# Kernel tuning notes

Measured on AMD Instinct MI355X. Metric: run time of the kernel, lower is better.

The kernel has to match this reference:

```python
import jax, jax.numpy as jnp
import numpy as np

N = 200000   # num atoms (nodes)
E = 400000   # one-way edges; symmetrized to 2E inside forward
H = 256      # hidden_dim == hidden_feats
LN_EPS = 1e-5


def setup_inputs() -> dict:
    key = jax.random.key(0)
    ks = jax.random.split(key, 48)
    def p(i, shape, s=0.05):
        return jax.random.normal(ks[i], shape, dtype=jnp.float32) * s
    inp = {
        'atom_inputs': jax.random.randint(ks[0], (N, 7), 0, 2),
        'src': jax.random.randint(ks[1], (E,), 0, N),
        'dst': jax.random.randint(ks[2], (E,), 0, N),
        # AtomEmbedding tables
        'emb_element': p(3, (100, 64)),
        'emb_degree': p(4, (7, 4)),
        'emb_valence': p(5, (7, 4)),
        'emb_charge': p(6, (8, 4)),
        'emb_aromatic': p(7, (2, 4)),
        'emb_hybrid': p(8, (6, 4)),
        'emb_hydrogen': p(9, (5, 4)),
        # linear_0: 88 -> H
        'W0': p(10, (88, H)), 'b0': jnp.zeros((H,), jnp.float32),
        # linear_1: H -> H
        'W1': p(11, (H, H)), 'b1': jnp.zeros((H,), jnp.float32),
    }
    # 4 GINEConv layers: node-MLP weight Wn/bn, edge Linear(1,H) weight We/be,
    # followed by LayerNorm gamma g / beta bt
    for i in range(4):
        inp[f'Wn{i}'] = p(12 + 4 * i, (H, H))
        inp[f'bn{i}'] = jnp.zeros((H,), jnp.float32)
        inp[f'We{i}'] = p(13 + 4 * i, (H,))
        inp[f'be{i}'] = jnp.zeros((H,), jnp.float32)
        inp[f'g{i}'] = jnp.ones((H,), jnp.float32)
        inp[f'bt{i}'] = jnp.zeros((H,), jnp.float32)
    return inp


def _layernorm(x, g, b):
    m = jnp.mean(x, axis=-1, keepdims=True)
    v = jnp.mean(jnp.square(x - m), axis=-1, keepdims=True)
    return (x - m) / jnp.sqrt(v + LN_EPS) * g + b


def reference(atom_inputs, src, dst,
              emb_element, emb_degree, emb_valence, emb_charge,
              emb_aromatic, emb_hybrid, emb_hydrogen,
              W0, b0, W1, b1,
              Wn0, bn0, We0, be0, g0, bt0,
              Wn1, bn1, We1, be1, g1, bt1,
              Wn2, bn2, We2, be2, g2, bt2,
              Wn3, bn3, We3, be3, g3, bt3):
    # --- AtomEmbedding: 7 lookups, concat -> [N, 88]
    feats = jnp.concatenate([
        emb_element[atom_inputs[:, 0]],
        emb_degree[atom_inputs[:, 1]],
        emb_valence[atom_inputs[:, 2] + 1],
        emb_charge[atom_inputs[:, 3]],
        emb_aromatic[atom_inputs[:, 4]],
        emb_hybrid[atom_inputs[:, 5]],
        emb_hydrogen[atom_inputs[:, 6]],
    ], axis=-1)
    h = feats @ W0 + b0  # [N, H]
    n = h.shape[0]

    # symmetrize edges: src||dst -> dst||src
    s = jnp.concatenate([src, dst])
    d = jnp.concatenate([dst, src])

    def gine(x, Wn, bn, We, be):
        # edge_attr is all-ones [2E,1]; Linear(1,H) applied to ones is the
        # constant vector We + be broadcast over edges.
        c = We + be                                   # [H]
        msg = jax.nn.relu(x[s] + c)                   # [2E, H] gather + add
        agg = jax.ops.segment_sum(msg, d, num_segments=n)  # scatter-sum
        return (x + agg) @ Wn + bn                    # eps=0: (1+eps)*x + agg

    h = _layernorm(gine(h, Wn0, bn0, We0, be0), g0, bt0)
    h = _layernorm(gine(h, Wn1, bn1, We1, be1), g1, bt1)
    h = _layernorm(gine(h, Wn2, bn2, We2, be2), g2, bt2)
    h = _layernorm(gine(h, Wn3, bn3, We3, be3), g3, bt3)
    return h @ W1 + b1
```

## Files before the change

kernel.cpp:

```cpp
#include <hip/hip_runtime.h>

#define HDIM 256

typedef __attribute__((ext_vector_type(8))) short short8;
typedef __attribute__((ext_vector_type(4))) float f32x4;

typedef const __attribute__((address_space(1))) unsigned int* gas_ptr;
typedef __attribute__((address_space(3))) unsigned int* las_ptr;

__device__ __forceinline__ unsigned short f2bf(float f) {
    unsigned int u = __float_as_uint(f);
    u += 0x7FFF + ((u >> 16) & 1);
    return (unsigned short)(u >> 16);
}
__device__ __forceinline__ float bf2f(unsigned short u) {
    return __uint_as_float(((unsigned int)u) << 16);
}


__global__ void k_zero_int(int* p, int n) {
    int i = blockIdx.x * blockDim.x + threadIdx.x;
    if (i < n) p[i] = 0;
}

__global__ void k_hist(const int* __restrict__ src, const int* __restrict__ dst,
                       int E, int* __restrict__ deg) {
    int e = blockIdx.x * blockDim.x + threadIdx.x;
    if (e >= E) return;
    atomicAdd(&deg[dst[e]], 1);
    atomicAdd(&deg[src[e]], 1);
}

__global__ void k_scan_partial(const int* __restrict__ deg, int* __restrict__ rp,
                               int* __restrict__ bsum, int n) {
    __shared__ int sd[256];
    int t = threadIdx.x;
    int base = blockIdx.x * 1024 + t * 4;
    int v[4]; int tsum = 0;
    #pragma unroll
    for (int k = 0; k < 4; k++) { v[k] = (base + k < n) ? deg[base + k] : 0; tsum += v[k]; }
    sd[t] = tsum; __syncthreads();
    for (int off = 1; off < 256; off <<= 1) {
        int x = (t >= off) ? sd[t - off] : 0;
        __syncthreads();
        sd[t] += x;
        __syncthreads();
    }
    int run = sd[t] - tsum;
    if (t == 255) bsum[blockIdx.x] = sd[255];
    #pragma unroll
    for (int k = 0; k < 4; k++) { if (base + k < n) rp[base + k] = run; run += v[k]; }
}

__global__ void k_scan_bsum(int* __restrict__ bsum, int nb) {
    __shared__ int sd[256];
    int t = threadIdx.x;
    int base = t * 4;
    int v[4]; int tsum = 0;
    #pragma unroll
    for (int k = 0; k < 4; k++) { v[k] = (base + k < nb) ? bsum[base + k] : 0; tsum += v[k]; }
    sd[t] = tsum; __syncthreads();
    for (int off = 1; off < 256; off <<= 1) {
        int x = (t >= off) ? sd[t - off] : 0;
        __syncthreads();
        sd[t] += x;
        __syncthreads();
    }
    int run = sd[t] - tsum;
    #pragma unroll
    for (int k = 0; k < 4; k++) { if (base + k < nb) bsum[base + k] = run; run += v[k]; }
}

__global__ void k_scan_add(int* __restrict__ rp, int* __restrict__ cursor,
                           const int* __restrict__ bsum, int n, int twoE) {
    int i = blockIdx.x * blockDim.x + threadIdx.x;
    if (i < n) {
        int v = rp[i] + bsum[i >> 10];
        rp[i] = v;
        cursor[i] = v;
    }
    if (i == 0) rp[n] = twoE;
}

__global__ void k_fill(const int* __restrict__ src, const int* __restrict__ dst,
                       int E, int* __restrict__ cursor, int* __restrict__ col) {
    int e = blockIdx.x * blockDim.x + threadIdx.x;
    if (e >= E) return;
    int s = src[e], d = dst[e];
    int p = atomicAdd(&cursor[d], 1); col[p] = s;
    int q = atomicAdd(&cursor[s], 1); col[q] = d;
}


__global__ void k_prep_w(const float* __restrict__ W, unsigned short* __restrict__ Wt) {
    int k = blockIdx.x, nn = threadIdx.x;
    Wt[nn * 256 + k] = f2bf(W[k * 256 + nn]);
}

__global__ void k_prep_w0(const float* __restrict__ W0, unsigned short* __restrict__ Wt0) {
    int k = blockIdx.x, nn = threadIdx.x;
    Wt0[nn * 96 + k] = (k < 88) ? f2bf(W0[k * 256 + nn]) : 0;
}


__global__ __launch_bounds__(256) void k_embed0(
    const int* __restrict__ atom,
    const float* __restrict__ eE, const float* __restrict__ eD,
    const float* __restrict__ eV, const float* __restrict__ eC,
    const float* __restrict__ eA, const float* __restrict__ eH,
    const float* __restrict__ eHy,
    const unsigned short* __restrict__ Wt0, const float* __restrict__ b0,
    unsigned short* __restrict__ x, int n) {
    __shared__ __align__(128) unsigned short As[64 * 256];
    int t = threadIdx.x;
    size_t node0 = (size_t)blockIdx.x * 64;

    {
        int row = t >> 2;
        int ks  = (t & 3) * 24;
        size_t node = node0 + row;
        int a0 = 0, a1 = 0, a2 = 0, a3 = 0, a4 = 0, a5 = 0, a6 = 0;
        bool ok = node < (size_t)n;
        if (ok) {
            const int* a = atom + node * 7;
            a0 = a[0]; a1 = a[1]; a2 = a[2]; a3 = a[3]; a4 = a[4]; a5 = a[5]; a6 = a[6];
        }
        #pragma unroll
        for (int kk = 0; kk < 24; kk++) {
            int k = ks + kk;
            float val = 0.f;
            if (ok) {
                if (k < 64)       val = eE[a0 * 64 + k];
                else if (k < 68)  val = eD[a1 * 4 + (k - 64)];
                else if (k < 72)  val = eV[(a2 + 1) * 4 + (k - 68)];
                else if (k < 76)  val = eC[a3 * 4 + (k - 72)];
                else if (k < 80)  val = eA[a4 * 4 + (k - 76)];
                else if (k < 84)  val = eH[a5 * 4 + (k - 80)];
                else if (k < 88)  val = eHy[a6 * 4 + (k - 84)];
            }
            int boff = (k * 2) ^ ((row & 7) << 4);
            *(unsigned short*)((char*)As + row * 256 + boff) = f2bf(val);
        }
    }
    __syncthreads();

    int w  = t >> 6;
    int l  = t & 63;
    int lr = l & 15;
    int lk = l >> 4;

    f32x4 acc[4][4];
    #pragma unroll
    for (int rg = 0; rg < 4; rg++)
        #pragma unroll
        for (int cg = 0; cg < 4; cg++)
            acc[rg][cg] = (f32x4){0.f, 0.f, 0.f, 0.f};

    #pragma unroll
    for (int kt = 0; kt < 3; kt++) {
        int kbyte = kt * 64 + lk * 16;
        short8 a[4], bf[4];
        #pragma unroll
        for (int rg = 0; rg < 4; rg++) {
            int row = rg * 16 + lr;
            a[rg] = *(const short8*)((const char*)As + row * 256 + (kbyte ^ ((row & 7) << 4)));
        }
        #pragma unroll
        for (int cg = 0; cg < 4; cg++) {
            int coln = w * 64 + cg * 16 + lr;
            bf[cg] = *(const short8*)((const char*)Wt0 + coln * 192 + kbyte);
        }
        #pragma unroll
        for (int rg = 0; rg < 4; rg++)
            #pragma unroll
            for (int cg = 0; cg < 4; cg++)
                acc[rg][cg] = __builtin_amdgcn_mfma_f32_16x16x32_bf16(a[rg], bf[cg], acc[rg][cg], 0, 0, 0);
    }

    float bcol[4];
    #pragma unroll
    for (int cg = 0; cg < 4; cg++) bcol[cg] = b0[w * 64 + cg * 16 + lr];

    __syncthreads();
    #pragma unroll
    for (int rg = 0; rg < 4; rg++)
        #pragma unroll
        for (int j = 0; j < 4; j++) {
            int row = rg * 16 + lk * 4 + j;
            #pragma unroll
            for (int cg = 0; cg < 4; cg++) {
                int colI = w * 64 + cg * 16 + lr;
                int byte = row * 512 + ((((colI >> 2) << 3) ^ ((row & 7) << 4)) + (colI & 3) * 2);
                *(unsigned short*)((char*)As + byte) = f2bf(acc[rg][cg][j] + bcol[cg]);
            }
        }
    __syncthreads();
    ushort4* xo = (ushort4*)(x + node0 * HDIM);
    #pragma unroll
    for (int i = 0; i < 16; i++) {
        int g4 = i * 256 + t;
        int row = g4 >> 6, c4 = g4 & 63;
        if (node0 + row < (size_t)n)
            xo[g4] = *(ushort4*)((char*)As + row * 512 + ((c4 << 3) ^ ((row & 7) << 4)));
    }
}


__global__ __launch_bounds__(256) void k_aggregate(
    const unsigned short* __restrict__ x, const int* __restrict__ rp,
    const int* __restrict__ col, const float* __restrict__ We,
    const float* __restrict__ be, unsigned short* __restrict__ z, int n) {
    int wid = threadIdx.x >> 6;
    int l   = threadIdx.x & 63;
    int h   = l >> 5;
    int j   = l & 31;
    int node = blockIdx.x * 8 + wid * 2 + h;
    bool ok = node < n;
    int nd = ok ? node : 0;
    const short8* x8 = (const short8*)x;

    float c[8];
    {
        float4 w0 = ((const float4*)We)[2 * j],     w1 = ((const float4*)We)[2 * j + 1];
        float4 e0 = ((const float4*)be)[2 * j],     e1 = ((const float4*)be)[2 * j + 1];
        c[0] = w0.x + e0.x; c[1] = w0.y + e0.y; c[2] = w0.z + e0.z; c[3] = w0.w + e0.w;
        c[4] = w1.x + e1.x; c[5] = w1.y + e1.y; c[6] = w1.z + e1.z; c[7] = w1.w + e1.w;
    }

    int p0 = rp[nd], p1 = rp[nd + 1];
    int deg = ok ? (p1 - p0) : 0;

    float acc[8];
    {
        short8 s = x8[(size_t)nd * 32 + j];
        #pragma unroll
        for (int k = 0; k < 8; k++) acc[k] = ok ? bf2f((unsigned short)s[k]) : 0.f;
    }

    for (int b = 0; b < deg; b += 32) {
        int m = deg - b; if (m > 32) m = 32;
        int idx = (j < m) ? col[p0 + b + j] : 0;
        int e = 0;
        for (; e + 2 <= m; e += 2) {
            int s0 = __shfl(idx, (h << 5) + e, 64);
            int s1 = __shfl(idx, (h << 5) + e + 1, 64);
            short8 u0 = x8[(size_t)s0 * 32 + j];
            short8 u1 = x8[(size_t)s1 * 32 + j];
            #pragma unroll
            for (int k = 0; k < 8; k++) acc[k] += fmaxf(bf2f((unsigned short)u0[k]) + c[k], 0.f);
            #pragma unroll
            for (int k = 0; k < 8; k++) acc[k] += fmaxf(bf2f((unsigned short)u1[k]) + c[k], 0.f);
        }
        if (e < m) {
            int s0 = __shfl(idx, (h << 5) + e, 64);
            short8 u0 = x8[(size_t)s0 * 32 + j];
            #pragma unroll
            for (int k = 0; k < 8; k++) acc[k] += fmaxf(bf2f((unsigned short)u0[k]) + c[k], 0.f);
        }
    }

    if (ok) {
        short8 o;
        #pragma unroll
        for (int k = 0; k < 8; k++) o[k] = (short)f2bf(acc[k]);
        ((short8*)z)[(size_t)nd * 32 + j] = o;
    }
}


template <bool DO_LN>
__global__ __launch_bounds__(256) void k_gemm_mfma(
    const unsigned short* __restrict__ zin, const unsigned short* __restrict__ Wt,
    const float* __restrict__ b, const float* __restrict__ g,
    const float* __restrict__ bt, void* __restrict__ xout_v, int n) {
    __shared__ __align__(128) unsigned short As[64 * 256];
    __shared__ float psum[4][64], psq[4][64];
    __shared__ float mean_s[64], inv_s[64];

    int t = threadIdx.x;
    int w = t >> 6;
    int l = t & 63;
    size_t node0 = (size_t)blockIdx.x * 64;

    if (node0 + 64 <= (size_t)n) {
        const char* ztile = (const char*)(zin + node0 * HDIM);
        #pragma unroll
        for (int it = 0; it < 8; it++) {
            int ldsbase = w * 8192 + it * 1024;
            int row = (ldsbase >> 9) + (l >> 5);
            int chunk = (l & 31) * 16;
            const char* src = ztile + row * 512 + (chunk ^ ((row & 7) << 4));
            __builtin_amdgcn_global_load_lds((gas_ptr)src,
                                             (las_ptr)((char*)As + ldsbase),
                                             16, 0, 0);
        }
    } else {
        const ushort4* zr = (const ushort4*)(zin + node0 * HDIM);
        #pragma unroll
        for (int i = 0; i < 16; i++) {
            int g4 = i * 256 + t;
            int row = g4 >> 6, c4 = g4 & 63;
            ushort4 v = make_ushort4(0, 0, 0, 0);
            if (node0 + row < (size_t)n) v = zr[g4];
            *(ushort4*)((char*)As + row * 512 + ((c4 << 3) ^ ((row & 7) << 4))) = v;
        }
    }
    __syncthreads();

    int lr = l & 15;
    int lk = l >> 4;

    f32x4 acc[4][4];
    #pragma unroll
    for (int rg = 0; rg < 4; rg++)
        #pragma unroll
        for (int cg = 0; cg < 4; cg++)
            acc[rg][cg] = (f32x4){0.f, 0.f, 0.f, 0.f};

    #pragma unroll
    for (int kt = 0; kt < 8; kt++) {
        int kbyte = kt * 64 + lk * 16;
        short8 a[4], bf[4];
        #pragma unroll
        for (int rg = 0; rg < 4; rg++) {
            int row = rg * 16 + lr;
            a[rg] = *(const short8*)((const char*)As + row * 512 + (kbyte ^ ((row & 7) << 4)));
        }
        #pragma unroll
        for (int cg = 0; cg < 4; cg++) {
            int coln = w * 64 + cg * 16 + lr;
            bf[cg] = *(const short8*)((const char*)Wt + coln * 512 + kbyte);
        }
        #pragma unroll
        for (int rg = 0; rg < 4; rg++)
            #pragma unroll
            for (int cg = 0; cg < 4; cg++)
                acc[rg][cg] = __builtin_amdgcn_mfma_f32_16x16x32_bf16(a[rg], bf[cg], acc[rg][cg], 0, 0, 0);
    }

    float bcol[4];
    #pragma unroll
    for (int cg = 0; cg < 4; cg++) bcol[cg] = b[w * 64 + cg * 16 + lr];
    #pragma unroll
    for (int rg = 0; rg < 4; rg++)
        #pragma unroll
        for (int cg = 0; cg < 4; cg++)
            #pragma unroll
            for (int j = 0; j < 4; j++) acc[rg][cg][j] += bcol[cg];

    if (!DO_LN) {
        float* xout = (float*)xout_v;
        #pragma unroll
        for (int rg = 0; rg < 4; rg++)
            #pragma unroll
            for (int j = 0; j < 4; j++) {
                int row = rg * 16 + lk * 4 + j;
                size_t node = node0 + row;
                if (node < (size_t)n) {
                    #pragma unroll
                    for (int cg = 0; cg < 4; cg++)
                        xout[node * HDIM + w * 64 + cg * 16 + lr] = acc[rg][cg][j];
                }
            }
        return;
    }

    float sv[4][4], sq[4][4];
    #pragma unroll
    for (int rg = 0; rg < 4; rg++)
        #pragma unroll
        for (int j = 0; j < 4; j++) {
            float s = 0.f, q = 0.f;
            #pragma unroll
            for (int cg = 0; cg < 4; cg++) {
                float v = acc[rg][cg][j];
                s += v; q += v * v;
            }
            sv[rg][j] = s; sq[rg][j] = q;
        }
    #pragma unroll
    for (int off = 1; off < 16; off <<= 1) {
        #pragma unroll
        for (int rg = 0; rg < 4; rg++)
            #pragma unroll
            for (int j = 0; j < 4; j++) {
                sv[rg][j] += __shfl_xor(sv[rg][j], off, 64);
                sq[rg][j] += __shfl_xor(sq[rg][j], off, 64);
            }
    }
    if (lr == 0) {
        #pragma unroll
        for (int rg = 0; rg < 4; rg++)
            #pragma unroll
            for (int j = 0; j < 4; j++) {
                int row = rg * 16 + lk * 4 + j;
                psum[w][row] = sv[rg][j];
                psq[w][row]  = sq[rg][j];
            }
    }
    __syncthreads();
    if (t < 64) {
        float s = psum[0][t] + psum[1][t] + psum[2][t] + psum[3][t];
        float q = psq[0][t] + psq[1][t] + psq[2][t] + psq[3][t];
        float m = s * (1.f / 256.f);
        float var = q * (1.f / 256.f) - m * m;
        mean_s[t] = m;
        inv_s[t]  = rsqrtf(var + 1e-5f);
    }
    __syncthreads();

    float gv[4], btv[4];
    #pragma unroll
    for (int cg = 0; cg < 4; cg++) {
        int coln = w * 64 + cg * 16 + lr;
        gv[cg] = g[coln]; btv[cg] = bt[coln];
    }
    #pragma unroll
    for (int rg = 0; rg < 4; rg++)
        #pragma unroll
        for (int j = 0; j < 4; j++) {
            int row = rg * 16 + lk * 4 + j;
            float m = mean_s[row];
            float inv = inv_s[row];
            #pragma unroll
            for (int cg = 0; cg < 4; cg++) {
                int colI = w * 64 + cg * 16 + lr;
                float v = (acc[rg][cg][j] - m) * inv * gv[cg] + btv[cg];
                int byte = row * 512 + ((((colI >> 2) << 3) ^ ((row & 7) << 4)) + (colI & 3) * 2);
                *(unsigned short*)((char*)As + byte) = f2bf(v);
            }
        }
    __syncthreads();
    ushort4* xo = (ushort4*)((unsigned short*)xout_v + node0 * HDIM);
    #pragma unroll
    for (int i = 0; i < 16; i++) {
        int g4 = i * 256 + t;
        int row = g4 >> 6, c4 = g4 & 63;
        if (node0 + row < (size_t)n)
            xo[g4] = *(ushort4*)((char*)As + row * 512 + ((c4 << 3) ^ ((row & 7) << 4)));
    }
}


extern "C" void kernel_launch(void* const* d_in, const int* in_sizes, int n_in,
                              void* d_out, int out_size, void* d_ws, size_t ws_size,
                              hipStream_t stream) {
    const int*   atom = (const int*)d_in[0];
    const int*   src  = (const int*)d_in[1];
    const int*   dst  = (const int*)d_in[2];
    const float* eE   = (const float*)d_in[3];
    const float* eD   = (const float*)d_in[4];
    const float* eV   = (const float*)d_in[5];
    const float* eC   = (const float*)d_in[6];
    const float* eA   = (const float*)d_in[7];
    const float* eH   = (const float*)d_in[8];
    const float* eHy  = (const float*)d_in[9];
    const float* W0   = (const float*)d_in[10];
    const float* b0   = (const float*)d_in[11];
    const float* W1   = (const float*)d_in[12];
    const float* b1   = (const float*)d_in[13];

    const int N = in_sizes[0] / 7;
    const int E = in_sizes[1];
    const int twoE = 2 * E;

    unsigned short* xb = (unsigned short*)d_ws;
    unsigned short* z  = xb + (size_t)N * HDIM;
    int*   rp      = (int*)(z + (size_t)N * HDIM);
    int*   cursor  = rp + (N + 1);
    int*   deg     = cursor + N;
    int*   col     = deg + N;
    int*   bsum    = col + twoE;
    uintptr_t pw = (uintptr_t)(bsum + 1024);
    pw = (pw + 255) & ~(uintptr_t)255;
    unsigned short* Wt  = (unsigned short*)pw;
    unsigned short* Wt0 = Wt + (size_t)5 * 65536;

    const int nb = (N + 1023) / 1024;

    k_zero_int<<<(N + 255) / 256, 256, 0, stream>>>(deg, N);
    k_hist<<<(E + 255) / 256, 256, 0, stream>>>(src, dst, E, deg);
    k_scan_partial<<<nb, 256, 0, stream>>>(deg, rp, bsum, N);
    k_scan_bsum<<<1, 256, 0, stream>>>(bsum, nb);
    k_scan_add<<<(N + 255) / 256, 256, 0, stream>>>(rp, cursor, bsum, N, twoE);
    k_fill<<<(E + 255) / 256, 256, 0, stream>>>(src, dst, E, cursor, col);

    for (int L = 0; L < 4; L++) {
        const float* Wn = (const float*)d_in[14 + 6 * L + 0];
        k_prep_w<<<256, 256, 0, stream>>>(Wn, Wt + (size_t)L * 65536);
    }
    k_prep_w<<<256, 256, 0, stream>>>(W1, Wt + (size_t)4 * 65536);
    k_prep_w0<<<96, 256, 0, stream>>>(W0, Wt0);

    const int nblk64 = (N + 63) / 64;
    const int nblk8  = (N + 7) / 8;

    k_embed0<<<nblk64, 256, 0, stream>>>(atom, eE, eD, eV, eC, eA, eH, eHy,
                                         Wt0, b0, xb, N);

    for (int L = 0; L < 4; L++) {
        const float* bn = (const float*)d_in[14 + 6 * L + 1];
        const float* We = (const float*)d_in[14 + 6 * L + 2];
        const float* be = (const float*)d_in[14 + 6 * L + 3];
        const float* g  = (const float*)d_in[14 + 6 * L + 4];
        const float* bt = (const float*)d_in[14 + 6 * L + 5];
        k_aggregate<<<nblk8, 256, 0, stream>>>(xb, rp, col, We, be, z, N);
        k_gemm_mfma<true><<<nblk64, 256, 0, stream>>>(z, Wt + (size_t)L * 65536,
                                                      bn, g, bt, xb, N);
    }

    k_gemm_mfma<false><<<nblk64, 256, 0, stream>>>(xb, Wt + (size_t)4 * 65536,
                                                   b1, nullptr, nullptr, d_out, N);
}
```

Before: 936.7 us.

## Fuse GINE aggregation with MFMA GEMM and LayerNorm into one kernel

Merges the per-layer edge aggregation kernel and the GEMM+LayerNorm kernel into a single 512-thread kernel. Each block aggregates 64 nodes into a swizzled LDS tile, then runs the MFMA GEMM against that tile and applies LayerNorm before writing bf16 output. Two buffers are ping-ponged between layers, so the z intermediate never makes a global write and read round trip. The cost is a larger block with a serial 4-nodes-per-half-wave gather loop, which may cut latency hiding and occupancy during the irregular gather phase. Weights are now loaded straight from global memory as the MFMA A operand.

```diff
diff --git a/kernel.cpp b/kernel.cpp
--- a/kernel.cpp
+++ b/kernel.cpp
@@ -206,76 +206,192 @@
 }
 
 
-__global__ __launch_bounds__(256) void k_aggregate(
+__global__ __launch_bounds__(512) void k_gine(
     const unsigned short* __restrict__ x, const int* __restrict__ rp,
     const int* __restrict__ col, const float* __restrict__ We,
-    const float* __restrict__ be, unsigned short* __restrict__ z, int n) {
-    int wid = threadIdx.x >> 6;
-    int l   = threadIdx.x & 63;
-    int h   = l >> 5;
-    int j   = l & 31;
-    int node = blockIdx.x * 8 + wid * 2 + h;
-    bool ok = node < n;
-    int nd = ok ? node : 0;
-    const short8* x8 = (const short8*)x;
-
-    float c[8];
+    const float* __restrict__ be, const unsigned short* __restrict__ Wt,
+    const float* __restrict__ b, const float* __restrict__ g,
+    const float* __restrict__ bt, unsigned short* __restrict__ xout, int n) {
+    __shared__ __align__(128) unsigned short As[64 * 256];
+    __shared__ float psum[8][64], psq[8][64];
+    __shared__ float mean_s[64], inv_s[64];
+
+    int t = threadIdx.x;
+    int wid = t >> 6;
+    int l = t & 63;
+    int h = l >> 5;
+    int j = l & 31;
+    size_t node0 = (size_t)blockIdx.x * 64;
+
     {
-        float4 w0 = ((const float4*)We)[2 * j],     w1 = ((const float4*)We)[2 * j + 1];
-        float4 e0 = ((const float4*)be)[2 * j],     e1 = ((const float4*)be)[2 * j + 1];
-        c[0] = w0.x + e0.x; c[1] = w0.y + e0.y; c[2] = w0.z + e0.z; c[3] = w0.w + e0.w;
-        c[4] = w1.x + e1.x; c[5] = w1.y + e1.y; c[6] = w1.z + e1.z; c[7] = w1.w + e1.w;
-    }
-
-    int p0 = rp[nd], p1 = rp[nd + 1];
-    int deg = ok ? (p1 - p0) : 0;
-
-    float acc[8];
-    {
-        short8 s = x8[(size_t)nd * 32 + j];
-        #pragma unroll
-        for (int k = 0; k < 8; k++) acc[k] = ok ? bf2f((unsigned short)s[k]) : 0.f;
-    }
-
-    for (int b = 0; b < deg; b += 32) {
-        int m = deg - b; if (m > 32) m = 32;
-        int idx = (j < m) ? col[p0 + b + j] : 0;
-        int e = 0;
-        for (; e + 2 <= m; e += 2) {
-            int s0 = __shfl(idx, (h << 5) + e, 64);
-            int s1 = __shfl(idx, (h << 5) + e + 1, 64);
-            short8 u0 = x8[(size_t)s0 * 32 + j];
-            short8 u1 = x8[(size_t)s1 * 32 + j];
-            #pragma unroll
-            for (int k = 0; k < 8; k++) acc[k] += fmaxf(bf2f((unsigned short)u0[k]) + c[k], 0.f);
-            #pragma unroll
-            for (int k = 0; k < 8; k++) acc[k] += fmaxf(bf2f((unsigned short)u1[k]) + c[k], 0.f);
-        }
-        if (e < m) {
-            int s0 = __shfl(idx, (h << 5) + e, 64);
-            short8 u0 = x8[(size_t)s0 * 32 + j];
-            #pragma unroll
-            for (int k = 0; k < 8; k++) acc[k] += fmaxf(bf2f((unsigned short)u0[k]) + c[k], 0.f);
-        }
-    }
-
-    if (ok) {
-        short8 o;
-        #pragma unroll
-        for (int k = 0; k < 8; k++) o[k] = (short)f2bf(acc[k]);
-        ((short8*)z)[(size_t)nd * 32 + j] = o;
-    }
-}
-
-
-template <bool DO_LN>
-__global__ __launch_bounds__(256) void k_gemm_mfma(
+        int hh = wid * 2 + h;
+        const short8* x8 = (const short8*)x;
+        float c[8];
+        {
+            float4 w0 = ((const float4*)We)[2 * j], w1 = ((const float4*)We)[2 * j + 1];
+            float4 e0 = ((const float4*)be)[2 * j], e1 = ((const float4*)be)[2 * j + 1];
+            c[0] = w0.x + e0.x; c[1] = w0.y + e0.y; c[2] = w0.z + e0.z; c[3] = w0.w + e0.w;
+            c[4] = w1.x + e1.x; c[5] = w1.y + e1.y; c[6] = w1.z + e1.z; c[7] = w1.w + e1.w;
+        }
+        for (int q = 0; q < 4; q++) {
+            int row = hh * 4 + q;
+            size_t node = node0 + row;
+            bool ok = node < (size_t)n;
+            int nd = ok ? (int)node : 0;
+            int p0 = rp[nd], p1 = rp[nd + 1];
+            int deg = ok ? (p1 - p0) : 0;
+
+            float acc[8];
+            short8 s = x8[(size_t)nd * 32 + j];
+            #pragma unroll
+            for (int k = 0; k < 8; k++) acc[k] = ok ? bf2f((unsigned short)s[k]) : 0.f;
+
+            for (int bb = 0; bb < deg; bb += 32) {
+                int m = deg - bb; if (m > 32) m = 32;
+                int idx = (j < m) ? col[p0 + bb + j] : 0;
+                int e = 0;
+                for (; e + 2 <= m; e += 2) {
+                    int s0 = __shfl(idx, (h << 5) + e, 64);
+                    int s1 = __shfl(idx, (h << 5) + e + 1, 64);
+                    short8 u0 = x8[(size_t)s0 * 32 + j];
+                    short8 u1 = x8[(size_t)s1 * 32 + j];
+                    #pragma unroll
+                    for (int k = 0; k < 8; k++) acc[k] += fmaxf(bf2f((unsigned short)u0[k]) + c[k], 0.f);
+                    #pragma unroll
+                    for (int k = 0; k < 8; k++) acc[k] += fmaxf(bf2f((unsigned short)u1[k]) + c[k], 0.f);
+                }
+                if (e < m) {
+                    int s0 = __shfl(idx, (h << 5) + e, 64);
+                    short8 u0 = x8[(size_t)s0 * 32 + j];
+                    #pragma unroll
+                    for (int k = 0; k < 8; k++) acc[k] += fmaxf(bf2f((unsigned short)u0[k]) + c[k], 0.f);
+                }
+            }
+
+            short8 o;
+            #pragma unroll
+            for (int k = 0; k < 8; k++) o[k] = (short)f2bf(acc[k]);
+            *(short8*)((char*)As + row * 512 + ((j ^ (row & 7)) << 4)) = o;
+        }
+    }
+    __syncthreads();
+
+    int lr = l & 15;
+    int lk = l >> 4;
+
+    f32x4 acc[2][4];
+    #pragma unroll
+    for (int fg = 0; fg < 2; fg++)
+        #pragma unroll
+        for (int ng = 0; ng < 4; ng++)
+            acc[fg][ng] = (f32x4){0.f, 0.f, 0.f, 0.f};
+
+    #pragma unroll
+    for (int kt = 0; kt < 8; kt++) {
+        int kbyte = kt * 64 + lk * 16;
+        short8 a[2], bfr[4];
+        #pragma unroll
+        for (int fg = 0; fg < 2; fg++) {
+            int feat = wid * 32 + fg * 16 + lr;
+            a[fg] = *(const short8*)((const char*)Wt + feat * 512 + kbyte);
+        }
+        #pragma unroll
+        for (int ng = 0; ng < 4; ng++) {
+            int row = ng * 16 + lr;
+            bfr[ng] = *(const short8*)((const char*)As + row * 512 + (kbyte ^ ((row & 7) << 4)));
+        }
+        #pragma unroll
+        for (int fg = 0; fg < 2; fg++)
+            #pragma unroll
+            for (int ng = 0; ng < 4; ng++)
+                acc[fg][ng] = __builtin_amdgcn_mfma_f32_16x16x32_bf16(a[fg], bfr[ng], acc[fg][ng], 0, 0, 0);
+    }
+
+    #pragma unroll
+    for (int fg = 0; fg < 2; fg++) {
+        float4 bv = *(const float4*)&b[wid * 32 + fg * 16 + 4 * lk];
+        #pragma unroll
+        for (int ng = 0; ng < 4; ng++) {
+            acc[fg][ng][0] += bv.x; acc[fg][ng][1] += bv.y;
+            acc[fg][ng][2] += bv.z; acc[fg][ng][3] += bv.w;
+        }
+    }
+
+    float sv[4], sq[4];
+    #pragma unroll
+    for (int ng = 0; ng < 4; ng++) {
+        float s = 0.f, q = 0.f;
+        #pragma unroll
+        for (int fg = 0; fg < 2; fg++)
+            #pragma unroll
+            for (int jj = 0; jj < 4; jj++) {
+                float v = acc[fg][ng][jj];
+                s += v; q += v * v;
+            }
+        sv[ng] = s; sq[ng] = q;
+    }
+    #pragma unroll
+    for (int ng = 0; ng < 4; ng++) {
+        sv[ng] += __shfl_xor(sv[ng], 16, 64);
+        sq[ng] += __shfl_xor(sq[ng], 16, 64);
+        sv[ng] += __shfl_xor(sv[ng], 32, 64);
+        sq[ng] += __shfl_xor(sq[ng], 32, 64);
+    }
+    if (lk == 0) {
+        #pragma unroll
+        for (int ng = 0; ng < 4; ng++) {
+            psum[wid][ng * 16 + lr] = sv[ng];
+            psq[wid][ng * 16 + lr]  = sq[ng];
+        }
+    }
+    __syncthreads();
+    if (t < 64) {
+        float s = 0.f, q = 0.f;
+        #pragma unroll
+        for (int wv = 0; wv < 8; wv++) { s += psum[wv][t]; q += psq[wv][t]; }
+        float m = s * (1.f / 256.f);
+        float var = q * (1.f / 256.f) - m * m;
+        mean_s[t] = m;
+        inv_s[t]  = rsqrtf(var + 1e-5f);
+    }
+    __syncthreads();
+
+    #pragma unroll
+    for (int fg = 0; fg < 2; fg++) {
+        int fbase = wid * 32 + fg * 16 + 4 * lk;
+        float4 gv  = *(const float4*)&g[fbase];
+        float4 btv = *(const float4*)&bt[fbase];
+        #pragma unroll
+        for (int ng = 0; ng < 4; ng++) {
+            int row = ng * 16 + lr;
+            float m = mean_s[row];
+            float inv = inv_s[row];
+            ushort4 h4;
+            h4.x = f2bf((acc[fg][ng][0] - m) * inv * gv.x + btv.x);
+            h4.y = f2bf((acc[fg][ng][1] - m) * inv * gv.y + btv.y);
+            h4.z = f2bf((acc[fg][ng][2] - m) * inv * gv.z + btv.z);
+            h4.w = f2bf((acc[fg][ng][3] - m) * inv * gv.w + btv.w);
+            int byte = row * 512 + ((fbase * 2) ^ ((row & 7) << 4));
+            *(ushort4*)((char*)As + byte) = h4;
+        }
+    }
+    __syncthreads();
+    #pragma unroll
+    for (int i = 0; i < 4; i++) {
+        int g16 = i * 512 + t;
+        int row = g16 >> 5, ch = g16 & 31;
+        if (node0 + row < (size_t)n) {
+            short8 v = *(const short8*)((const char*)As + row * 512 + ((ch ^ (row & 7)) << 4));
+            ((short8*)xout)[(node0 + row) * 32 + ch] = v;
+        }
+    }
+}
+
+
+__global__ __launch_bounds__(256) void k_gemm_final(
     const unsigned short* __restrict__ zin, const unsigned short* __restrict__ Wt,
-    const float* __restrict__ b, const float* __restrict__ g,
-    const float* __restrict__ bt, void* __restrict__ xout_v, int n) {
+    const float* __restrict__ b, float* __restrict__ xout, int n) {
     __shared__ __align__(128) unsigned short As[64 * 256];
-    __shared__ float psum[4][64], psq[4][64];
-    __shared__ float mean_s[64], inv_s[64];
 
     int t = threadIdx.x;
     int w = t >> 6;
@@ -344,101 +460,15 @@
     #pragma unroll
     for (int rg = 0; rg < 4; rg++)
         #pragma unroll
-        for (int cg = 0; cg < 4; cg++)
-            #pragma unroll
-            for (int j = 0; j < 4; j++) acc[rg][cg][j] += bcol[cg];
-
-    if (!DO_LN) {
-        float* xout = (float*)xout_v;
-        #pragma unroll
-        for (int rg = 0; rg < 4; rg++)
-            #pragma unroll
-            for (int j = 0; j < 4; j++) {
-                int row = rg * 16 + lk * 4 + j;
-                size_t node = node0 + row;
-                if (node < (size_t)n) {
-                    #pragma unroll
-                    for (int cg = 0; cg < 4; cg++)
-                        xout[node * HDIM + w * 64 + cg * 16 + lr] = acc[rg][cg][j];
-                }
-            }
-        return;
-    }
-
-    float sv[4][4], sq[4][4];
-    #pragma unroll
-    for (int rg = 0; rg < 4; rg++)
-        #pragma unroll
-        for (int j = 0; j < 4; j++) {
-            float s = 0.f, q = 0.f;
-            #pragma unroll
-            for (int cg = 0; cg < 4; cg++) {
-                float v = acc[rg][cg][j];
-                s += v; q += v * v;
-            }
-            sv[rg][j] = s; sq[rg][j] = q;
-        }
-    #pragma unroll
-    for (int off = 1; off < 16; off <<= 1) {
-        #pragma unroll
-        for (int rg = 0; rg < 4; rg++)
-            #pragma unroll
-            for (int j = 0; j < 4; j++) {
-                sv[rg][j] += __shfl_xor(sv[rg][j], off, 64);
-                sq[rg][j] += __shfl_xor(sq[rg][j], off, 64);
-            }
-    }
-    if (lr == 0) {
-        #pragma unroll
-        for (int rg = 0; rg < 4; rg++)
-            #pragma unroll
-            for (int j = 0; j < 4; j++) {
-                int row = rg * 16 + lk * 4 + j;
-                psum[w][row] = sv[rg][j];
-                psq[w][row]  = sq[rg][j];
-            }
-    }
-    __syncthreads();
-    if (t < 64) {
-        float s = psum[0][t] + psum[1][t] + psum[2][t] + psum[3][t];
-        float q = psq[0][t] + psq[1][t] + psq[2][t] + psq[3][t];
-        float m = s * (1.f / 256.f);
-        float var = q * (1.f / 256.f) - m * m;
-        mean_s[t] = m;
-        inv_s[t]  = rsqrtf(var + 1e-5f);
-    }
-    __syncthreads();
-
-    float gv[4], btv[4];
-    #pragma unroll
-    for (int cg = 0; cg < 4; cg++) {
-        int coln = w * 64 + cg * 16 + lr;
-        gv[cg] = g[coln]; btv[cg] = bt[coln];
-    }
-    #pragma unroll
-    for (int rg = 0; rg < 4; rg++)
-        #pragma unroll
         for (int j = 0; j < 4; j++) {
             int row = rg * 16 + lk * 4 + j;
-            float m = mean_s[row];
-            float inv = inv_s[row];
-            #pragma unroll
-            for (int cg = 0; cg < 4; cg++) {
-                int colI = w * 64 + cg * 16 + lr;
-                float v = (acc[rg][cg][j] - m) * inv * gv[cg] + btv[cg];
-                int byte = row * 512 + ((((colI >> 2) << 3) ^ ((row & 7) << 4)) + (colI & 3) * 2);
-                *(unsigned short*)((char*)As + byte) = f2bf(v);
+            size_t node = node0 + row;
+            if (node < (size_t)n) {
+                #pragma unroll
+                for (int cg = 0; cg < 4; cg++)
+                    xout[node * HDIM + w * 64 + cg * 16 + lr] = acc[rg][cg][j] + bcol[cg];
             }
         }
-    __syncthreads();
-    ushort4* xo = (ushort4*)((unsigned short*)xout_v + node0 * HDIM);
-    #pragma unroll
-    for (int i = 0; i < 16; i++) {
-        int g4 = i * 256 + t;
-        int row = g4 >> 6, c4 = g4 & 63;
-        if (node0 + row < (size_t)n)
-            xo[g4] = *(ushort4*)((char*)As + row * 512 + ((c4 << 3) ^ ((row & 7) << 4)));
-    }
 }
 
 
@@ -493,22 +523,23 @@
     k_prep_w0<<<96, 256, 0, stream>>>(W0, Wt0);
 
     const int nblk64 = (N + 63) / 64;
-    const int nblk8  = (N + 7) / 8;
 
     k_embed0<<<nblk64, 256, 0, stream>>>(atom, eE, eD, eV, eC, eA, eH, eHy,
                                          Wt0, b0, xb, N);
 
+    unsigned short* cur = xb;
+    unsigned short* nxt = z;
     for (int L = 0; L < 4; L++) {
         const float* bn = (const float*)d_in[14 + 6 * L + 1];
         const float* We = (const float*)d_in[14 + 6 * L + 2];
         const float* be = (const float*)d_in[14 + 6 * L + 3];
-        const float* g  = (const float*)d_in[14 + 6 * L + 4];
+        const float* gg = (const float*)d_in[14 + 6 * L + 4];
         const float* bt = (const float*)d_in[14 + 6 * L + 5];
-        k_aggregate<<<nblk8, 256, 0, stream>>>(xb, rp, col, We, be, z, N);
-        k_gemm_mfma<true><<<nblk64, 256, 0, stream>>>(z, Wt + (size_t)L * 65536,
-                                                      bn, g, bt, xb, N);
-    }
-
-    k_gemm_mfma<false><<<nblk64, 256, 0, stream>>>(xb, Wt + (size_t)4 * 65536,
-                                                   b1, nullptr, nullptr, d_out, N);
-}
+        k_gine<<<nblk64, 512, 0, stream>>>(cur, rp, col, We, be,
+                                           Wt + (size_t)L * 65536, bn, gg, bt, nxt, N);
+        unsigned short* tmp = cur; cur = nxt; nxt = tmp;
+    }
+
+    k_gemm_final<<<nblk64, 256, 0, stream>>>(cur, Wt + (size_t)4 * 65536,
+                                             b1, (float*)d_out, N);
+}
```

Result: faster. 794.0 us (-15.2%).
